# Performance work log

Measured on AMD Instinct MI355X. Metric: run time of the kernel, lower is better.

Reference implementation:

```python
import jax, jax.numpy as jnp
import numpy as np

IN_FEATURES = 1024
NUM_EXPERTS = 64
TOP_K = 2


def setup_inputs() -> dict:
    key = jax.random.key(0)
    kx, kw, kb = jax.random.split(key, 3)
    x = jax.random.normal(kx, (8, 4096, IN_FEATURES), dtype=jnp.float32)
    # nn.Linear init scale ~ 1/sqrt(in_features)
    bound = 1.0 / np.sqrt(IN_FEATURES)
    W = jax.random.uniform(kw, (NUM_EXPERTS, IN_FEATURES), dtype=jnp.float32, minval=-bound, maxval=bound)
    b = jax.random.uniform(kb, (NUM_EXPERTS,), dtype=jnp.float32, minval=-bound, maxval=bound)
    return {"x": x, "W": W, "b": b}


def reference(x, W, b):
    # logits: [B, S, E]
    logits = jnp.einsum("bsd,ed->bse", x, W) + b
    gates = jax.nn.softmax(logits, axis=-1)
    top_k_gates, top_k_indices = jax.lax.top_k(gates, TOP_K)
    return top_k_gates, top_k_indices
```

## Files before the change

### kernel.cpp

```cpp
#include <hip/hip_runtime.h>
#include <hip/hip_bf16.h>

#define D 1024
#define E 64
#define TPB 256
#define TOKS 64
#define KC 64
#define BROW 72

typedef __attribute__((ext_vector_type(8))) short bf16x8;
typedef __attribute__((ext_vector_type(4))) float f32x4;
typedef __attribute__((ext_vector_type(4))) int i32x4;
typedef __attribute__((ext_vector_type(4))) unsigned short u16x4;

__device__ __forceinline__ unsigned short bf16_rne(float f) {
    unsigned u = __builtin_bit_cast(unsigned, f);
    u += 0x7fffu + ((u >> 16) & 1u);
    return (unsigned short)(u >> 16);
}
__device__ __forceinline__ float bf16_as_f(unsigned short h) {
    unsigned u = ((unsigned)h) << 16;
    return __builtin_bit_cast(float, u);
}
__device__ __forceinline__ void split_hi_lo(float v, unsigned short& h, unsigned short& l) {
    h = bf16_rne(v);
    l = bf16_rne(v - bf16_as_f(h));
}

__global__ __launch_bounds__(256) void wsplit_kernel(const float* __restrict__ W,
        unsigned short* __restrict__ whi, unsigned short* __restrict__ wlo) {
    int g = blockIdx.x * 256 + threadIdx.x;
    f32x4 w = *(const f32x4*)(W + (size_t)g * 4);
    u16x4 h, l;
#pragma unroll
    for (int j = 0; j < 4; ++j) {
        unsigned short hh, ll;
        split_hi_lo(w[j], hh, ll);
        h[j] = hh; l[j] = ll;
    }
    *(u16x4*)(whi + (size_t)g * 4) = h;
    *(u16x4*)(wlo + (size_t)g * 4) = l;
}

__global__ __launch_bounds__(TPB) void router_kernel(
        const float* __restrict__ x,
        const unsigned short* __restrict__ whi,
        const unsigned short* __restrict__ wlo,
        const float* __restrict__ bias,
        float* __restrict__ out, int T) {
    __shared__ __align__(16) union SM {
        struct { unsigned short hi[E][BROW]; unsigned short lo[E][BROW]; } b;
        float ls[TOKS][E + 1];
    } sm;
    __shared__ float sbias[E];

    const int tid  = threadIdx.x;
    const int lane = tid & 63;
    const int wid  = tid >> 6;
    const int n    = lane & 15;
    const int q    = lane >> 4;
    const int t0   = blockIdx.x * TOKS;

    if (tid < E) sbias[tid] = bias[tid];

    f32x4 acc[4];
#pragma unroll
    for (int i = 0; i < 4; ++i) acc[i] = (f32x4){0.f, 0.f, 0.f, 0.f};

    const float* arow = x + (size_t)(t0 + wid * 16 + n) * D + q * 8;

    i32x4 wreg[4];
    auto load_w = [&](int kc) {
#pragma unroll
        for (int r = 0; r < 4; ++r) {
            int idx = ((r & 1) << 8) + tid;
            int e = idx >> 3, blk = idx & 7;
            const unsigned short* src = (r >> 1) ? wlo : whi;
            wreg[r] = *(const i32x4*)(src + (size_t)e * D + kc + blk * 8);
        }
    };
    auto store_w = [&]() {
#pragma unroll
        for (int r = 0; r < 4; ++r) {
            int idx = ((r & 1) << 8) + tid;
            int e = idx >> 3, blk = idx & 7;
            unsigned short* dst = (r >> 1) ? &sm.b.lo[e][blk * 8] : &sm.b.hi[e][blk * 8];
            *(i32x4*)dst = wreg[r];
        }
    };

    load_w(0);
    f32x4 areg[4];
#pragma unroll
    for (int s = 0; s < 2; ++s) {
        areg[2 * s]     = *(const f32x4*)(arow + s * 32);
        areg[2 * s + 1] = *(const f32x4*)(arow + s * 32 + 4);
    }

    for (int kc = 0; kc < D; kc += KC) {
        store_w();
        __syncthreads();

        int kn = (kc + KC) & (D - 1);
        load_w(kn);
        f32x4 anext[4];
#pragma unroll
        for (int s = 0; s < 2; ++s) {
            anext[2 * s]     = *(const f32x4*)(arow + kn + s * 32);
            anext[2 * s + 1] = *(const f32x4*)(arow + kn + s * 32 + 4);
        }

#pragma unroll
        for (int s = 0; s < 2; ++s) {
            unsigned short ah[8], al[8];
#pragma unroll
            for (int j = 0; j < 4; ++j) {
                split_hi_lo(areg[2 * s][j],     ah[j],     al[j]);
                split_hi_lo(areg[2 * s + 1][j], ah[4 + j], al[4 + j]);
            }
            bf16x8 ahv, alv;
#pragma unroll
            for (int j = 0; j < 8; ++j) { ahv[j] = (short)ah[j]; alv[j] = (short)al[j]; }
#pragma unroll
            for (int nt = 0; nt < 4; ++nt) {
                const bf16x8 bh = *(const bf16x8*)&sm.b.hi[nt * 16 + n][s * 32 + q * 8];
                const bf16x8 bl = *(const bf16x8*)&sm.b.lo[nt * 16 + n][s * 32 + q * 8];
                acc[nt] = __builtin_amdgcn_mfma_f32_16x16x32_bf16(ahv, bh, acc[nt], 0, 0, 0);
                acc[nt] = __builtin_amdgcn_mfma_f32_16x16x32_bf16(alv, bh, acc[nt], 0, 0, 0);
                acc[nt] = __builtin_amdgcn_mfma_f32_16x16x32_bf16(ahv, bl, acc[nt], 0, 0, 0);
            }
        }
#pragma unroll
        for (int i = 0; i < 4; ++i) areg[i] = anext[i];
        __syncthreads();
    }

#pragma unroll
    for (int nt = 0; nt < 4; ++nt) {
        int col = nt * 16 + n;
        float bv = sbias[col];
#pragma unroll
        for (int r = 0; r < 4; ++r) {
            sm.ls[wid * 16 + q * 4 + r][col] = acc[nt][r] + bv;
        }
    }
    __syncthreads();

    if (tid < TOKS) {
        float m1 = -3.4e38f, m2 = -3.4e38f;
        int i1 = 0, i2 = 0;
        for (int e = 0; e < E; ++e) {
            float v = sm.ls[tid][e];
            if (v > m1) { m2 = m1; i2 = i1; m1 = v; i1 = e; }
            else if (v > m2) { m2 = v; i2 = e; }
        }
        float Z = 0.f;
        for (int e = 0; e < E; ++e) Z += __expf(sm.ls[tid][e] - m1);
        float inv = 1.f / Z;
        int gt = t0 + tid;
        out[(size_t)gt * 2]     = inv;
        out[(size_t)gt * 2 + 1] = __expf(m2 - m1) * inv;
        float* oi = out + (size_t)T * 2;
        oi[(size_t)gt * 2]     = (float)i1;
        oi[(size_t)gt * 2 + 1] = (float)i2;
    }
}

extern "C" void kernel_launch(void* const* d_in, const int* in_sizes, int n_in,
                              void* d_out, int out_size, void* d_ws, size_t ws_size,
                              hipStream_t stream) {
    const float* x = (const float*)d_in[0];
    const float* W = (const float*)d_in[1];
    const float* b = (const float*)d_in[2];
    float* out = (float*)d_out;
    unsigned short* whi = (unsigned short*)d_ws;
    unsigned short* wlo = whi + (size_t)E * D;
    int T = in_sizes[0] / D;
    hipLaunchKernelGGL(wsplit_kernel, dim3((E * D) / 1024), dim3(256), 0, stream,
                       W, whi, wlo);
    hipLaunchKernelGGL(router_kernel, dim3(T / TOKS), dim3(TPB), 0, stream,
                       x, whi, wlo, b, out, T);
}
```

Measured before the change: 210.4 us.

## Load router weight fragments directly from global into registers, drop LDS staging

Each wave now loads its bf16 hi/lo weight fragments straight from global memory (L2-resident, 256KB total) into registers in MFMA layout, removing the shared-memory staging buffer and both per-chunk __syncthreads. Bias is folded into the accumulator initialisation and launch bounds request two blocks per CU. This trades LDS traffic and barriers for four-fold redundant global/L2 weight reads across waves and more registers, with the weight load no longer prefetched a chunk ahead.

```diff
diff --git a/kernel.cpp b/kernel.cpp
--- a/kernel.cpp
+++ b/kernel.cpp
@@ -6,7 +6,7 @@
 #define TPB 256
 #define TOKS 64
 #define KC 64
-#define BROW 72
+#define NCHUNK (D / KC)
 
 typedef __attribute__((ext_vector_type(8))) short bf16x8;
 typedef __attribute__((ext_vector_type(4))) float f32x4;
@@ -42,17 +42,13 @@
     *(u16x4*)(wlo + (size_t)g * 4) = l;
 }
 
-__global__ __launch_bounds__(TPB) void router_kernel(
+__global__ __launch_bounds__(TPB, 2) void router_kernel(
         const float* __restrict__ x,
         const unsigned short* __restrict__ whi,
         const unsigned short* __restrict__ wlo,
         const float* __restrict__ bias,
         float* __restrict__ out, int T) {
-    __shared__ __align__(16) union SM {
-        struct { unsigned short hi[E][BROW]; unsigned short lo[E][BROW]; } b;
-        float ls[TOKS][E + 1];
-    } sm;
-    __shared__ float sbias[E];
+    __shared__ float ls[TOKS][E + 1];
 
     const int tid  = threadIdx.x;
     const int lane = tid & 63;
@@ -61,87 +57,74 @@
     const int q    = lane >> 4;
     const int t0   = blockIdx.x * TOKS;
 
-    if (tid < E) sbias[tid] = bias[tid];
-
     f32x4 acc[4];
 #pragma unroll
-    for (int i = 0; i < 4; ++i) acc[i] = (f32x4){0.f, 0.f, 0.f, 0.f};
+    for (int nt = 0; nt < 4; ++nt) {
+        float bv = bias[nt * 16 + n];
+        acc[nt] = (f32x4){bv, bv, bv, bv};
+    }
 
     const float* arow = x + (size_t)(t0 + wid * 16 + n) * D + q * 8;
+    size_t brow[4];
+#pragma unroll
+    for (int nt = 0; nt < 4; ++nt) brow[nt] = (size_t)(nt * 16 + n) * D + q * 8;
 
-    i32x4 wreg[4];
-    auto load_w = [&](int kc) {
+    i32x4 breg[4][2][2];
+    f32x4 aregA[4], aregB[4];
+
+    auto load_b = [&](int c) {
 #pragma unroll
-        for (int r = 0; r < 4; ++r) {
-            int idx = ((r & 1) << 8) + tid;
-            int e = idx >> 3, blk = idx & 7;
-            const unsigned short* src = (r >> 1) ? wlo : whi;
-            wreg[r] = *(const i32x4*)(src + (size_t)e * D + kc + blk * 8);
-        }
+        for (int nt = 0; nt < 4; ++nt)
+#pragma unroll
+            for (int s = 0; s < 2; ++s) {
+                breg[nt][s][0] = *(const i32x4*)(whi + brow[nt] + c * KC + s * 32);
+                breg[nt][s][1] = *(const i32x4*)(wlo + brow[nt] + c * KC + s * 32);
+            }
     };
-    auto store_w = [&]() {
+    auto load_a = [&](int c, f32x4* ar) {
 #pragma unroll
-        for (int r = 0; r < 4; ++r) {
-            int idx = ((r & 1) << 8) + tid;
-            int e = idx >> 3, blk = idx & 7;
-            unsigned short* dst = (r >> 1) ? &sm.b.lo[e][blk * 8] : &sm.b.hi[e][blk * 8];
-            *(i32x4*)dst = wreg[r];
+        for (int s = 0; s < 2; ++s) {
+            ar[2 * s]     = *(const f32x4*)(arow + c * KC + s * 32);
+            ar[2 * s + 1] = *(const f32x4*)(arow + c * KC + s * 32 + 4);
         }
     };
 
-    load_w(0);
-    f32x4 areg[4];
-#pragma unroll
-    for (int s = 0; s < 2; ++s) {
-        areg[2 * s]     = *(const f32x4*)(arow + s * 32);
-        areg[2 * s + 1] = *(const f32x4*)(arow + s * 32 + 4);
-    }
+    load_a(0, aregA);
 
-    for (int kc = 0; kc < D; kc += KC) {
-        store_w();
-        __syncthreads();
-
-        int kn = (kc + KC) & (D - 1);
-        load_w(kn);
-        f32x4 anext[4];
-#pragma unroll
-        for (int s = 0; s < 2; ++s) {
-            anext[2 * s]     = *(const f32x4*)(arow + kn + s * 32);
-            anext[2 * s + 1] = *(const f32x4*)(arow + kn + s * 32 + 4);
-        }
+    for (int kc = 0; kc < NCHUNK; ++kc) {
+        load_b(kc);
+        int kn = (kc + 1) & (NCHUNK - 1);
+        load_a(kn, aregB);
 
 #pragma unroll
         for (int s = 0; s < 2; ++s) {
             unsigned short ah[8], al[8];
 #pragma unroll
             for (int j = 0; j < 4; ++j) {
-                split_hi_lo(areg[2 * s][j],     ah[j],     al[j]);
-                split_hi_lo(areg[2 * s + 1][j], ah[4 + j], al[4 + j]);
+                split_hi_lo(aregA[2 * s][j],     ah[j],     al[j]);
+                split_hi_lo(aregA[2 * s + 1][j], ah[4 + j], al[4 + j]);
             }
             bf16x8 ahv, alv;
 #pragma unroll
             for (int j = 0; j < 8; ++j) { ahv[j] = (short)ah[j]; alv[j] = (short)al[j]; }
 #pragma unroll
             for (int nt = 0; nt < 4; ++nt) {
-                const bf16x8 bh = *(const bf16x8*)&sm.b.hi[nt * 16 + n][s * 32 + q * 8];
-                const bf16x8 bl = *(const bf16x8*)&sm.b.lo[nt * 16 + n][s * 32 + q * 8];
+                const bf16x8 bh = __builtin_bit_cast(bf16x8, breg[nt][s][0]);
+                const bf16x8 bl = __builtin_bit_cast(bf16x8, breg[nt][s][1]);
                 acc[nt] = __builtin_amdgcn_mfma_f32_16x16x32_bf16(ahv, bh, acc[nt], 0, 0, 0);
                 acc[nt] = __builtin_amdgcn_mfma_f32_16x16x32_bf16(alv, bh, acc[nt], 0, 0, 0);
                 acc[nt] = __builtin_amdgcn_mfma_f32_16x16x32_bf16(ahv, bl, acc[nt], 0, 0, 0);
             }
         }
 #pragma unroll
-        for (int i = 0; i < 4; ++i) areg[i] = anext[i];
-        __syncthreads();
+        for (int i = 0; i < 4; ++i) aregA[i] = aregB[i];
     }
 
 #pragma unroll
     for (int nt = 0; nt < 4; ++nt) {
-        int col = nt * 16 + n;
-        float bv = sbias[col];
 #pragma unroll
         for (int r = 0; r < 4; ++r) {
-            sm.ls[wid * 16 + q * 4 + r][col] = acc[nt][r] + bv;
+            ls[wid * 16 + q * 4 + r][nt * 16 + n] = acc[nt][r];
         }
     }
     __syncthreads();
@@ -150,12 +133,12 @@
         float m1 = -3.4e38f, m2 = -3.4e38f;
         int i1 = 0, i2 = 0;
         for (int e = 0; e < E; ++e) {
-            float v = sm.ls[tid][e];
+            float v = ls[tid][e];
             if (v > m1) { m2 = m1; i2 = i1; m1 = v; i1 = e; }
             else if (v > m2) { m2 = v; i2 = e; }
         }
         float Z = 0.f;
-        for (int e = 0; e < E; ++e) Z += __expf(sm.ls[tid][e] - m1);
+        for (int e = 0; e < E; ++e) Z += __expf(ls[tid][e] - m1);
         float inv = 1.f / Z;
         int gt = t0 + tid;
         out[(size_t)gt * 2]     = inv;
```

Result: slower. 239.5 us (+13.8%).
